# Performance work log

Measured on AMD Instinct MI355X. Metric: run time of the kernel, lower is better.

## Reference

```python
import jax, jax.numpy as jnp
import numpy as np

N = 100000      # num nodes
E = 1600000     # random edges
F_IN = 128      # n_features
H1, H2 = 128, 64   # gnns_forward_hidden
FC1, C = 128, 10   # linears_hidden[-1], n_classes
M = 20000       # masked nodes
SLOPE = 0.2     # LeakyReLU negative slope (GATConv default)


def _glorot(key, shape):
    fan = shape[0]
    return jax.random.normal(key, shape, dtype=jnp.float32) / jnp.sqrt(jnp.float32(fan))


def setup_inputs() -> dict:
    key = jax.random.key(0)
    ks = jax.random.split(key, 16)
    x = jax.random.normal(ks[0], (N, F_IN), dtype=jnp.float32)
    edge_index = jax.random.randint(ks[1], (2, E), 0, N, dtype=jnp.int64)
    mask = jax.random.randint(ks[2], (M,), 0, N, dtype=jnp.int64)
    return {
        "x": x, "edge_index": edge_index, "mask": mask,
        # GAT layer 1: F_IN -> H1
        "W1": _glorot(ks[3], (F_IN, H1)),
        "a_src1": _glorot(ks[4], (H1,)), "a_dst1": _glorot(ks[5], (H1,)),
        "b1": jnp.zeros((H1,), jnp.float32),
        # GAT layer 2: H1 -> H2
        "W2": _glorot(ks[6], (H1, H2)),
        "a_src2": _glorot(ks[7], (H2,)), "a_dst2": _glorot(ks[8], (H2,)),
        "b2": jnp.zeros((H2,), jnp.float32),
        # FC head: H2 -> FC1 -> C
        "fc1_w": _glorot(ks[9], (H2, FC1)), "fc1_b": jnp.zeros((FC1,), jnp.float32),
        "fc2_w": _glorot(ks[10], (FC1, C)), "fc2_b": jnp.zeros((C,), jnp.float32),
    }


def _gat_layer(x, src, dst, W, a_src, a_dst, b):
    h = x @ W                                   # [N, F_out]
    alpha_s = h @ a_src                         # [N]
    alpha_d = h @ a_dst                         # [N]
    e = jax.nn.leaky_relu(alpha_s[src] + alpha_d[dst], SLOPE)  # [E+N]
    # segment softmax over incoming edges of each destination node
    m = jax.ops.segment_max(e, dst, num_segments=N)            # self-loops guarantee non-empty
    w = jnp.exp(e - m[dst])
    z = jax.ops.segment_sum(w, dst, num_segments=N)
    attn = w / z[dst]                           # [E+N]
    out = jax.ops.segment_sum(attn[:, None] * h[src], dst, num_segments=N)
    return out + b


def reference(x, edge_index, mask, W1, a_src1, a_dst1, b1, W2, a_src2, a_dst2, b2, fc1_w, fc1_b, fc2_w, fc2_b):
    loops = jnp.arange(N, dtype=edge_index.dtype)
    src = jnp.concatenate([edge_index[0], loops])   # random edges + self loops (norm_adj adds I)
    dst = jnp.concatenate([edge_index[1], loops])
    h = jax.nn.relu(_gat_layer(x, src, dst, W1, a_src1, a_dst1, b1))   # GATBlock 1 (eval: no dropout/BN)
    h = jax.nn.relu(_gat_layer(h, src, dst, W2, a_src2, a_dst2, b2))   # GATBlock 2
    hm = h[mask]                                    # x[mask] on last layer output
    z = jax.nn.relu(hm @ fc1_w + fc1_b)             # FCsBlock hidden layer
    return z @ fc2_w + fc2_b                        # logits [M, C]
```

## Files before the change

### kernel.cpp

```cpp
#include <hip/hip_runtime.h>
#include <hip/hip_bf16.h>

constexpr int kN    = 100000;
constexpr int kE    = 1600000;
constexpr int kTotE = kE + kN;
constexpr int kM    = 20000;
constexpr float kSlope = 0.2f;

constexpr int kNB   = (kN + 127) >> 7;
constexpr int kBCap = 3072;
constexpr int kEB   = 4096;
constexpr int kSB   = (kTotE + kEB - 1) / kEB;
constexpr int kG1B  = (kN / 16 + 3) / 4;

typedef short short8  __attribute__((ext_vector_type(8)));
typedef float floatx4 __attribute__((ext_vector_type(4)));
typedef float floatx2 __attribute__((ext_vector_type(2)));

__device__ __forceinline__ float bf2f(unsigned short u) {
  union { unsigned int i; float f; } v; v.i = ((unsigned int)u) << 16; return v.f;
}
__device__ __forceinline__ floatx2 ubf2(unsigned int v) {
  union { unsigned int u; float f; } lo, hi;
  lo.u = v << 16; hi.u = v & 0xffff0000u;
  floatx2 r; r.x = lo.f; r.y = hi.f; return r;
}
__device__ __forceinline__ unsigned int packbf2(float lo, float hi) {
  __hip_bfloat162 h = __float22bfloat162_rn(float2{lo, hi});
  union { __hip_bfloat162 v; unsigned int u; } c; c.v = h; return c.u;
}
__device__ __forceinline__ unsigned short f2bf1(float f) {
  return (unsigned short)(packbf2(f, f) & 0xffffu);
}
__device__ __forceinline__ short8 pack8(float4 u, float4 v) {
  union { short8 s; unsigned int w[4]; } r;
  r.w[0] = packbf2(u.x, u.y); r.w[1] = packbf2(u.z, u.w);
  r.w[2] = packbf2(v.x, v.y); r.w[3] = packbf2(v.z, v.w);
  return r.s;
}

__device__ __forceinline__ void wprep1(int idx, const float* W, unsigned short* Wf,
                                       int Fo) {
  int j    = idx & 7;
  int lane = (idx >> 3) & 63;
  int t    = idx >> 9;
  int NT = Fo >> 4;
  int kt = t / NT, nt = t - kt * NT;
  int k = kt * 32 + ((lane >> 4) & 3) * 8 + j;
  int n = nt * 16 + (lane & 15);
  Wf[idx] = f2bf1(W[k * Fo + n]);
}

__global__ __launch_bounds__(256) void k_setup(const float* __restrict__ W1,
                                               const float* __restrict__ W2,
                                               const float* __restrict__ fc1w,
                                               unsigned short* __restrict__ Wf1,
                                               unsigned short* __restrict__ Wf2,
                                               unsigned short* __restrict__ Wf3,
                                               int* __restrict__ bcursor) {
  int gid = blockIdx.x * 256 + threadIdx.x;
  if (gid < kNB) bcursor[gid] = 0;
  if (gid < 16384)      wprep1(gid,          W1,   Wf1, 128);
  else if (gid < 24576) wprep1(gid - 16384,  W2,   Wf2, 64);
  else if (gid < 32768) wprep1(gid - 24576,  fc1w, Wf3, 128);
}

__global__ __launch_bounds__(256) void k_sg1(const int* __restrict__ esrc,
                                             const int* __restrict__ edst,
                                             int* __restrict__ bucketCursor,
                                             int* __restrict__ pairs,
                                             const float* __restrict__ x,
                                             const unsigned short* __restrict__ Wf,
                                             const float* __restrict__ asrc,
                                             const float* __restrict__ adst,
                                             unsigned short* __restrict__ h1,
                                             float* __restrict__ as, float* __restrict__ ad) {
  __shared__ int smemi[4096];
  int t = threadIdx.x;
  if (blockIdx.x < kSB) {
    int* hist    = smemi;
    int* runBase = smemi + kNB;
    int* binCur  = smemi + 2 * kNB;
    int b = blockIdx.x;
    for (int i = t; i < kNB; i += 256) hist[i] = 0;
    __syncthreads();
    int i0 = b * kEB;
#pragma unroll
    for (int k = 0; k < kEB / 256; ++k) {
      int i = i0 + t + k * 256;
      if (i < kTotE) {
        int d = (i < kE) ? edst[i] : (i - kE);
        atomicAdd(&hist[d >> 7], 1);
      }
    }
    __syncthreads();
    for (int i = t; i < kNB; i += 256) {
      int c = hist[i];
      int base = -1;
      if (c) {
        base = atomicAdd(&bucketCursor[i], c);
        if (base + c > kBCap) base = -1;
      }
      runBase[i] = base;
      binCur[i] = 0;
    }
    __syncthreads();
#pragma unroll
    for (int k = 0; k < kEB / 256; ++k) {
      int i = i0 + t + k * 256;
      if (i < kTotE) {
        int s, d;
        if (i < kE) { s = esrc[i]; d = edst[i]; }
        else        { s = d = i - kE; }
        int bin = d >> 7;
        int lp = atomicAdd(&binCur[bin], 1);
        int rb = runBase[bin];
        if (rb >= 0) pairs[(size_t)bin * kBCap + rb + lp] = ((d & 127) << 17) | s;
      }
    }
    return;
  }
  int wave = t >> 6, lane = t & 63;
  int strip = (blockIdx.x - kSB) * 4 + wave;
  if (strip >= kN / 16) return;
  int r0 = strip * 16;
  int m = lane & 15, quad = lane >> 4;
  const float4* xf = (const float4*)(x + (size_t)(r0 + m) * 128);
  short8 a0 = pack8(xf[quad * 2 + 0],  xf[quad * 2 + 1]);
  short8 a1 = pack8(xf[quad * 2 + 8],  xf[quad * 2 + 9]);
  short8 a2 = pack8(xf[quad * 2 + 16], xf[quad * 2 + 17]);
  short8 a3 = pack8(xf[quad * 2 + 24], xf[quad * 2 + 25]);
  const short8* wf = (const short8*)Wf;
  floatx4 acc[8];
#pragma unroll
  for (int nt = 0; nt < 8; ++nt) acc[nt] = floatx4{0.f, 0.f, 0.f, 0.f};
#pragma unroll
  for (int nt = 0; nt < 8; ++nt) {
    acc[nt] = __builtin_amdgcn_mfma_f32_16x16x32_bf16(a0, wf[(0 * 8 + nt) * 64 + lane], acc[nt], 0, 0, 0);
    acc[nt] = __builtin_amdgcn_mfma_f32_16x16x32_bf16(a1, wf[(1 * 8 + nt) * 64 + lane], acc[nt], 0, 0, 0);
    acc[nt] = __builtin_amdgcn_mfma_f32_16x16x32_bf16(a2, wf[(2 * 8 + nt) * 64 + lane], acc[nt], 0, 0, 0);
    acc[nt] = __builtin_amdgcn_mfma_f32_16x16x32_bf16(a3, wf[(3 * 8 + nt) * 64 + lane], acc[nt], 0, 0, 0);
  }
#pragma unroll
  for (int reg = 0; reg < 4; ++reg) {
    float s = 0.f, d = 0.f;
#pragma unroll
    for (int nt = 0; nt < 8; ++nt) {
      float v = acc[nt][reg];
      s += v * asrc[nt * 16 + m];
      d += v * adst[nt * 16 + m];
    }
#pragma unroll
    for (int off = 1; off < 16; off <<= 1) { s += __shfl_xor(s, off); d += __shfl_xor(d, off); }
    if (m == 0) { as[r0 + quad * 4 + reg] = s; ad[r0 + quad * 4 + reg] = d; }
  }
  unsigned short* tw = (unsigned short*)smemi + wave * 2048;
#pragma unroll
  for (int nt = 0; nt < 8; ++nt)
#pragma unroll
    for (int reg = 0; reg < 4; ++reg)
      tw[(quad * 4 + reg) * 128 + nt * 16 + m] = f2bf1(acc[nt][reg]);
  asm volatile("s_waitcnt lgkmcnt(0)" ::: "memory");
  const short8* tr = (const short8*)tw;
  short8* dstp = (short8*)(h1 + (size_t)r0 * 128);
#pragma unroll
  for (int sweep = 0; sweep < 4; ++sweep)
    dstp[sweep * 64 + lane] = tr[sweep * 64 + lane];
}

__global__ __launch_bounds__(256) void k_bucket_csr(int* __restrict__ pairs,
                                                    const int* __restrict__ bucketCursor,
                                                    int* __restrict__ rstart,
                                                    int* __restrict__ degA) {
  __shared__ int pl[kBCap];
  __shared__ int colLDS[kBCap];
  __shared__ int nhist[128], nstart[128], ncur[128], scanbuf[128];
  int b = blockIdx.x, t = threadIdx.x;
  int cnt  = min(bucketCursor[b], kBCap);
  int base = b * kBCap;
  if (t < 128) { nhist[t] = 0; ncur[t] = 0; }
  __syncthreads();
  for (int j = t; j < cnt; j += 256) {
    int p = pairs[(size_t)base + j];
    pl[j] = p;
    atomicAdd(&nhist[(p >> 17) & 127], 1);
  }
  __syncthreads();
  if (t < 128) scanbuf[t] = nhist[t];
  __syncthreads();
  for (int off = 1; off < 128; off <<= 1) {
    int u = (t < 128 && t >= off) ? scanbuf[t - off] : 0;
    __syncthreads();
    if (t < 128) scanbuf[t] += u;
    __syncthreads();
  }
  if (t < 128) nstart[t] = scanbuf[t] - nhist[t];
  __syncthreads();
  int nodes = min(128, kN - b * 128);
  if (t < nodes) {
    rstart[b * 128 + t] = base + nstart[t];
    degA[b * 128 + t]   = nhist[t];
  }
  for (int j = t; j < cnt; j += 256) {
    int p = pl[j];
    int nl = (p >> 17) & 127;
    int lp = atomicAdd(&ncur[nl], 1);
    colLDS[nstart[nl] + lp] = p & 0x1FFFF;
  }
  __syncthreads();
  for (int j = t; j < cnt; j += 256)
    pairs[(size_t)base + j] = colLDS[j];
}

__global__ __launch_bounds__(256) void k_gemm2(const unsigned short* __restrict__ o1,
                                               const unsigned short* __restrict__ Wf,
                                               const float* __restrict__ asrc,
                                               const float* __restrict__ adst,
                                               unsigned short* __restrict__ h2,
                                               float* __restrict__ as, float* __restrict__ ad) {
  __shared__ unsigned short tile[4][16 * 64];
  int wave = threadIdx.x >> 6, lane = threadIdx.x & 63;
  int strip = blockIdx.x * 4 + wave;
  if (strip >= kN / 16) return;
  int r0 = strip * 16;
  int m = lane & 15, quad = lane >> 4;
  const short8* xs = (const short8*)(o1 + (size_t)(r0 + m) * 128);
  short8 a0 = xs[quad], a1 = xs[quad + 4], a2 = xs[quad + 8], a3 = xs[quad + 12];
  const short8* wf = (const short8*)Wf;
  floatx4 acc[4];
#pragma unroll
  for (int nt = 0; nt < 4; ++nt) acc[nt] = floatx4{0.f, 0.f, 0.f, 0.f};
#pragma unroll
  for (int nt = 0; nt < 4; ++nt) {
    acc[nt] = __builtin_amdgcn_mfma_f32_16x16x32_bf16(a0, wf[(0 * 4 + nt) * 64 + lane], acc[nt], 0, 0, 0);
    acc[nt] = __builtin_amdgcn_mfma_f32_16x16x32_bf16(a1, wf[(1 * 4 + nt) * 64 + lane], acc[nt], 0, 0, 0);
    acc[nt] = __builtin_amdgcn_mfma_f32_16x16x32_bf16(a2, wf[(2 * 4 + nt) * 64 + lane], acc[nt], 0, 0, 0);
    acc[nt] = __builtin_amdgcn_mfma_f32_16x16x32_bf16(a3, wf[(3 * 4 + nt) * 64 + lane], acc[nt], 0, 0, 0);
  }
#pragma unroll
  for (int reg = 0; reg < 4; ++reg) {
    float s = 0.f, d = 0.f;
#pragma unroll
    for (int nt = 0; nt < 4; ++nt) {
      float v = acc[nt][reg];
      s += v * asrc[nt * 16 + m];
      d += v * adst[nt * 16 + m];
    }
#pragma unroll
    for (int off = 1; off < 16; off <<= 1) { s += __shfl_xor(s, off); d += __shfl_xor(d, off); }
    if (m == 0) { as[r0 + quad * 4 + reg] = s; ad[r0 + quad * 4 + reg] = d; }
  }
  unsigned short* tw = tile[wave];
#pragma unroll
  for (int nt = 0; nt < 4; ++nt)
#pragma unroll
    for (int reg = 0; reg < 4; ++reg)
      tw[(quad * 4 + reg) * 64 + nt * 16 + m] = f2bf1(acc[nt][reg]);
  asm volatile("s_waitcnt lgkmcnt(0)" ::: "memory");
  const short8* tr = (const short8*)tw;
  short8* dstp = (short8*)(h2 + (size_t)r0 * 64);
#pragma unroll
  for (int sweep = 0; sweep < 2; ++sweep)
    dstp[sweep * 64 + lane] = tr[sweep * 64 + lane];
}

template <int F, bool MASKED>
__global__ __launch_bounds__(256) void k_agg(const unsigned short* __restrict__ h,
                                             const int* __restrict__ rstart,
                                             const int* __restrict__ degA,
                                             const int* __restrict__ col,
                                             const float* __restrict__ as,
                                             const float* __restrict__ ad,
                                             const float* __restrict__ bias,
                                             unsigned short* __restrict__ out,
                                             const int* __restrict__ maskIdx) {
  __shared__ int2 swb[4][64];
  int wave = threadIdx.x >> 6, lane = threadIdx.x & 63;
  int idx = blockIdx.x * 4 + wave;
  if (idx >= (MASKED ? kM : kN)) return;
  int n = MASKED ? maskIdx[idx] : idx;
  int nout = MASKED ? idx : n;
  int beg = rstart[n];
  int deg = degA[n];
  float adn = ad[n];

  if (deg <= 64) {
    int j = beg + lane;
    int boff = 0; float e = -1e30f;
    if (lane < deg) {
      int s = col[j];
      boff = s << (F == 128 ? 8 : 7);
      float t = as[s] + adn;
      e = t > 0.f ? t : kSlope * t;
    }
    float mx = e;
#pragma unroll
    for (int off = 32; off; off >>= 1) mx = fmaxf(mx, __shfl_xor(mx, off));
    float w0 = __expf(e - mx);
    float l = w0;
#pragma unroll
    for (int off = 32; off; off >>= 1) l += __shfl_xor(l, off);
    float w = w0 * (1.f / l);
    floatx2 ax0{0.f, 0.f}, ax1{0.f, 0.f}, ax2{0.f, 0.f}, ax3{0.f, 0.f};
    const char* hb = (const char*)h;
    if (F == 128) {
      int quarter = lane >> 4, ql = lane & 15;
      int cnt8 = (deg + 7) & ~7;
#pragma unroll 2
      for (int k = 0; k < cnt8; k += 8) {
        int i1 = k + quarter, i2 = i1 + 4;
        int   b1 = __shfl(boff, i1), b2 = __shfl(boff, i2);
        float w1 = __shfl(w, i1),    w2 = __shfl(w, i2);
        uint4 v1 = *(const uint4*)(hb + b1 + ql * 16);
        uint4 v2 = *(const uint4*)(hb + b2 + ql * 16);
        floatx2 wv1{w1, w1}, wv2{w2, w2};
        ax0 += wv1 * ubf2(v1.x); ax1 += wv1 * ubf2(v1.y);
        ax2 += wv1 * ubf2(v1.z); ax3 += wv1 * ubf2(v1.w);
        ax0 += wv2 * ubf2(v2.x); ax1 += wv2 * ubf2(v2.y);
        ax2 += wv2 * ubf2(v2.z); ax3 += wv2 * ubf2(v2.w);
      }
      float a[8] = {ax0.x, ax0.y, ax1.x, ax1.y, ax2.x, ax2.y, ax3.x, ax3.y};
#pragma unroll
      for (int i = 0; i < 8; ++i) {
        a[i] += __shfl_xor(a[i], 16);
        a[i] += __shfl_xor(a[i], 32);
      }
      if (quarter == 0) {
        float4 b0 = ((const float4*)bias)[ql * 2];
        float4 b1 = ((const float4*)bias)[ql * 2 + 1];
        uint4 pk;
        pk.x = packbf2(fmaxf(a[0] + b0.x, 0.f), fmaxf(a[1] + b0.y, 0.f));
        pk.y = packbf2(fmaxf(a[2] + b0.z, 0.f), fmaxf(a[3] + b0.w, 0.f));
        pk.z = packbf2(fmaxf(a[4] + b1.x, 0.f), fmaxf(a[5] + b1.y, 0.f));
        pk.w = packbf2(fmaxf(a[6] + b1.z, 0.f), fmaxf(a[7] + b1.w, 0.f));
        ((uint4*)(out + (size_t)nout * 128))[ql] = pk;
      }
    } else {
      int eighth = lane >> 3, el = lane & 7;
      int cnt16 = (deg + 15) & ~15;
#pragma unroll 2
      for (int k = 0; k < cnt16; k += 16) {
        int i1 = k + eighth, i2 = i1 + 8;
        int   b1 = __shfl(boff, i1), b2 = __shfl(boff, i2);
        float w1 = __shfl(w, i1),    w2 = __shfl(w, i2);
        uint4 v1 = *(const uint4*)(hb + b1 + el * 16);
        uint4 v2 = *(const uint4*)(hb + b2 + el * 16);
        floatx2 wv1{w1, w1}, wv2{w2, w2};
        ax0 += wv1 * ubf2(v1.x); ax1 += wv1 * ubf2(v1.y);
        ax2 += wv1 * ubf2(v1.z); ax3 += wv1 * ubf2(v1.w);
        ax0 += wv2 * ubf2(v2.x); ax1 += wv2 * ubf2(v2.y);
        ax2 += wv2 * ubf2(v2.z); ax3 += wv2 * ubf2(v2.w);
      }
      float a[8] = {ax0.x, ax0.y, ax1.x, ax1.y, ax2.x, ax2.y, ax3.x, ax3.y};
#pragma unroll
      for (int i = 0; i < 8; ++i) {
        a[i] += __shfl_xor(a[i], 8);
        a[i] += __shfl_xor(a[i], 16);
        a[i] += __shfl_xor(a[i], 32);
      }
      if (eighth == 0) {
        float4 b0 = ((const float4*)bias)[el * 2];
        float4 b1 = ((const float4*)bias)[el * 2 + 1];
        uint4 pk;
        pk.x = packbf2(fmaxf(a[0] + b0.x, 0.f), fmaxf(a[1] + b0.y, 0.f));
        pk.y = packbf2(fmaxf(a[2] + b0.z, 0.f), fmaxf(a[3] + b0.w, 0.f));
        pk.z = packbf2(fmaxf(a[4] + b1.x, 0.f), fmaxf(a[5] + b1.y, 0.f));
        pk.w = packbf2(fmaxf(a[6] + b1.z, 0.f), fmaxf(a[7] + b1.w, 0.f));
        ((uint4*)(out + (size_t)nout * 64))[el] = pk;
      }
    }
    return;
  }

  int end = beg + deg;
  float m = -1e30f, l = 0.f;
  for (int j0 = beg; j0 < end; j0 += 64) {
    int j = j0 + lane;
    float e = -1e30f;
    if (j < end) {
      int s = col[j];
      float t = as[s] + adn;
      e = t > 0.f ? t : kSlope * t;
    }
    float cm = e;
#pragma unroll
    for (int off = 32; off; off >>= 1) cm = fmaxf(cm, __shfl_xor(cm, off));
    float w = __expf(e - cm);
    float cl = w;
#pragma unroll
    for (int off = 32; off; off >>= 1) cl += __shfl_xor(cl, off);
    float mn = fmaxf(m, cm);
    l = l * __expf(m - mn) + cl * __expf(cm - mn);
    m = mn;
  }
  float invl = 1.f / l;
  float a0 = 0.f, a1 = 0.f;
  int half = lane >> 5, hl = lane & 31;
  for (int j0 = beg; j0 < end; j0 += 64) {
    asm volatile("s_waitcnt lgkmcnt(0)" ::: "memory");
    int j = j0 + lane;
    if (j < end) {
      int s = col[j];
      float t = as[s] + adn;
      float e = t > 0.f ? t : kSlope * t;
      float w = __expf(e - m) * invl;
      swb[wave][lane] = int2{s, (int)__float_as_int(w)};
    }
    asm volatile("s_waitcnt lgkmcnt(0)" ::: "memory");
    int cntc = min(64, end - j0);
    if (F == 128) {
      for (int k = 0; k < cntc; ++k) {
        int2 p = swb[wave][k];
        float w = __int_as_float(p.y);
        unsigned int v = ((const unsigned int*)(h + (size_t)p.x * 128))[lane];
        a0 += w * bf2f((unsigned short)(v & 0xffffu));
        a1 += w * bf2f((unsigned short)(v >> 16));
      }
    } else {
      for (int k = 0; k < cntc; k += 2) {
        int kk = k + half;
        if (kk < cntc) {
          int2 p = swb[wave][kk];
          float w = __int_as_float(p.y);
          unsigned int v = ((const unsigned int*)(h + (size_t)p.x * 64))[hl];
          a0 += w * bf2f((unsigned short)(v & 0xffffu));
          a1 += w * bf2f((unsigned short)(v >> 16));
        }
      }
    }
  }
  if (F == 128) {
    float o0 = fmaxf(a0 + bias[2 * lane], 0.f);
    float o1 = fmaxf(a1 + bias[2 * lane + 1], 0.f);
    ((unsigned int*)(out + (size_t)nout * 128))[lane] = packbf2(o0, o1);
  } else {
    a0 += __shfl_xor(a0, 32);
    a1 += __shfl_xor(a1, 32);
    if (half == 0) {
      float o0 = fmaxf(a0 + bias[2 * hl], 0.f);
      float o1 = fmaxf(a1 + bias[2 * hl + 1], 0.f);
      ((unsigned int*)(out + (size_t)nout * 64))[hl] = packbf2(o0, o1);
    }
  }
}

__global__ __launch_bounds__(256) void k_fc(const unsigned short* __restrict__ o2m,
                                            const unsigned short* __restrict__ Wf,
                                            const float* __restrict__ fc1b,
                                            const float* __restrict__ fc2w,
                                            const float* __restrict__ fc2b,
                                            float* __restrict__ out) {
  __shared__ unsigned short tile[4][16 * 128];
  int wave = threadIdx.x >> 6, lane = threadIdx.x & 63;
  int strip = blockIdx.x * 4 + wave;
  if (strip >= kM / 16) return;
  int r0 = strip * 16;
  int m = lane & 15, quad = lane >> 4;
  const short8* xs = (const short8*)(o2m + (size_t)(r0 + m) * 64);
  short8 a0 = xs[quad], a1 = xs[quad + 4];
  const short8* wf = (const short8*)Wf;
  floatx4 acc[8];
#pragma unroll
  for (int nt = 0; nt < 8; ++nt) acc[nt] = floatx4{0.f, 0.f, 0.f, 0.f};
#pragma unroll
  for (int nt = 0; nt < 8; ++nt) {
    acc[nt] = __builtin_amdgcn_mfma_f32_16x16x32_bf16(a0, wf[(0 * 8 + nt) * 64 + lane], acc[nt], 0, 0, 0);
    acc[nt] = __builtin_amdgcn_mfma_f32_16x16x32_bf16(a1, wf[(1 * 8 + nt) * 64 + lane], acc[nt], 0, 0, 0);
  }
  unsigned short* tw = tile[wave];
#pragma unroll
  for (int nt = 0; nt < 8; ++nt) {
    float bb = fc1b[nt * 16 + m];
#pragma unroll
    for (int reg = 0; reg < 4; ++reg)
      tw[(quad * 4 + reg) * 128 + nt * 16 + m] = f2bf1(fmaxf(acc[nt][reg] + bb, 0.f));
  }
  asm volatile("s_waitcnt lgkmcnt(0)" ::: "memory");
  int c = lane & 15, q = lane >> 4;
  bool active = c < 10;
  float wreg[32];
#pragma unroll
  for (int i = 0; i < 32; ++i)
    wreg[i] = active ? fc2w[(q * 32 + i) * 10 + c] : 0.f;
  float bc = active ? fc2b[c] : 0.f;
  for (int r = 0; r < 16; ++r) {
    const uint2* zr = (const uint2*)(tw + r * 128 + q * 32);
    float acc2 = 0.f;
#pragma unroll
    for (int i = 0; i < 8; ++i) {
      uint2 v = zr[i];
      acc2 += bf2f((unsigned short)(v.x & 0xffffu)) * wreg[4 * i]
            + bf2f((unsigned short)(v.x >> 16))     * wreg[4 * i + 1]
            + bf2f((unsigned short)(v.y & 0xffffu)) * wreg[4 * i + 2]
            + bf2f((unsigned short)(v.y >> 16))     * wreg[4 * i + 3];
    }
    acc2 += __shfl_xor(acc2, 16);
    acc2 += __shfl_xor(acc2, 32);
    if (q == 0 && active) out[(size_t)(r0 + r) * 10 + c] = acc2 + bc;
  }
}

extern "C" void kernel_launch(void* const* d_in, const int* in_sizes, int n_in,
                              void* d_out, int out_size, void* d_ws, size_t ws_size,
                              hipStream_t stream) {
  const float* x     = (const float*)d_in[0];
  const int*   ei    = (const int*)d_in[1];
  const int*   mask  = (const int*)d_in[2];
  const float* W1    = (const float*)d_in[3];
  const float* asrc1 = (const float*)d_in[4];
  const float* adst1 = (const float*)d_in[5];
  const float* b1    = (const float*)d_in[6];
  const float* W2    = (const float*)d_in[7];
  const float* asrc2 = (const float*)d_in[8];
  const float* adst2 = (const float*)d_in[9];
  const float* b2    = (const float*)d_in[10];
  const float* fc1w  = (const float*)d_in[11];
  const float* fc1b  = (const float*)d_in[12];
  const float* fc2w  = (const float*)d_in[13];
  const float* fc2b  = (const float*)d_in[14];
  float* out = (float*)d_out;

  const int* esrc = ei;
  const int* edst = ei + kE;

  char* ws = (char*)d_ws;
  size_t off = 0;
  auto alloc = [&](size_t bytes) -> void* {
    void* p = ws + off;
    off = (off + bytes + 255) & ~(size_t)255;
    return p;
  };
  unsigned short* Wf1     = (unsigned short*)alloc(128 * 128 * 2);
  unsigned short* Wf2     = (unsigned short*)alloc(128 * 64 * 2);
  unsigned short* Wf3     = (unsigned short*)alloc(64 * 128 * 2);
  int*            rstart  = (int*)alloc((size_t)kN * 4);
  int*            degA    = (int*)alloc((size_t)kN * 4);
  int*            bcursor = (int*)alloc((size_t)kNB * 4);
  float*          as1     = (float*)alloc((size_t)kN * 4);
  float*          ad1     = (float*)alloc((size_t)kN * 4);
  float*          as2     = (float*)alloc((size_t)kN * 4);
  float*          ad2     = (float*)alloc((size_t)kN * 4);
  int*            pairs   = (int*)alloc((size_t)kNB * kBCap * 4);
  unsigned short* h1      = (unsigned short*)alloc((size_t)kN * 128 * 2);
  unsigned short* o1      = (unsigned short*)alloc((size_t)kN * 128 * 2);
  unsigned short* h2  = h1;
  unsigned short* o2m = h1 + (size_t)kN * 64;
  (void)ws_size; (void)in_sizes; (void)n_in; (void)out_size;

  const int nodeBlocks = (kN + 3) / 4;
  const int maskBlocks = (kM + 3) / 4;

  k_setup<<<128, 256, 0, stream>>>(W1, W2, fc1w, Wf1, Wf2, Wf3, bcursor);
  k_sg1<<<kSB + kG1B, 256, 0, stream>>>(esrc, edst, bcursor, pairs,
                                        x, Wf1, asrc1, adst1, h1, as1, ad1);
  k_bucket_csr<<<kNB, 256, 0, stream>>>(pairs, bcursor, rstart, degA);
  k_agg<128, false><<<nodeBlocks, 256, 0, stream>>>(h1, rstart, degA, pairs,
                                                    as1, ad1, b1, o1, nullptr);
  k_gemm2<<<kG1B, 256, 0, stream>>>(o1, Wf2, asrc2, adst2, h2, as2, ad2);
  k_agg<64, true><<<maskBlocks, 256, 0, stream>>>(h2, rstart, degA, pairs,
                                                  as2, ad2, b2, o2m, mask);
  k_fc<<<(kM / 16 + 3) / 4, 256, 0, stream>>>(o2m, Wf3, fc1b, fc2w, fc2b, out);
}
```

Baseline: 266.6 us.

## Slice layer-1 features into column blocks and precompute softmax weights in CSR build

The layer-1 GEMM now writes h1 in a sliced layout: 8 feature slices of 16 bf16 each, stored contiguously across nodes. A new slice-parallel aggregation kernel gathers only 32 bytes per edge per block, which aims to keep each slice's working set cache-resident during the random gather. The per-edge attention softmax for layer 1 moves into the bucket CSR kernel, computed serially per node into a new weights buffer. Each edge's col and weight are then re-read eight times, and the softmax runs one thread per node, which risks load imbalance and extra memory traffic.

```diff
diff --git a/kernel.cpp b/kernel.cpp
--- a/kernel.cpp
+++ b/kernel.cpp
@@ -162,16 +162,23 @@
       tw[(quad * 4 + reg) * 128 + nt * 16 + m] = f2bf1(acc[nt][reg]);
   asm volatile("s_waitcnt lgkmcnt(0)" ::: "memory");
   const short8* tr = (const short8*)tw;
-  short8* dstp = (short8*)(h1 + (size_t)r0 * 128);
-#pragma unroll
-  for (int sweep = 0; sweep < 4; ++sweep)
-    dstp[sweep * 64 + lane] = tr[sweep * 64 + lane];
+  short8* h8 = (short8*)h1;
+#pragma unroll
+  for (int sweep = 0; sweep < 4; ++sweep) {
+    int i8 = sweep * 64 + lane;
+    int row = i8 >> 4, e8 = i8 & 15;
+    int slice = e8 >> 1, half = e8 & 1;
+    h8[((size_t)slice * kN + (r0 + row)) * 2 + half] = tr[i8];
+  }
 }
 
 __global__ __launch_bounds__(256) void k_bucket_csr(int* __restrict__ pairs,
                                                     const int* __restrict__ bucketCursor,
                                                     int* __restrict__ rstart,
-                                                    int* __restrict__ degA) {
+                                                    int* __restrict__ degA,
+                                                    const float* __restrict__ as1,
+                                                    const float* __restrict__ ad1,
+                                                    float* __restrict__ wts) {
   __shared__ int pl[kBCap];
   __shared__ int colLDS[kBCap];
   __shared__ int nhist[128], nstart[128], ncur[128], scanbuf[128];
@@ -210,6 +217,66 @@
   __syncthreads();
   for (int j = t; j < cnt; j += 256)
     pairs[(size_t)base + j] = colLDS[j];
+  float* eLDS = (float*)pl;
+  if (t < nodes) {
+    int st = nstart[t], dg = nhist[t];
+    float adn = ad1[b * 128 + t];
+    float mx = -1e30f;
+    for (int i = 0; i < dg; ++i) {
+      int s = colLDS[st + i];
+      float tt = as1[s] + adn;
+      float e = tt > 0.f ? tt : kSlope * tt;
+      eLDS[st + i] = e;
+      mx = fmaxf(mx, e);
+    }
+    float sum = 0.f;
+    for (int i = 0; i < dg; ++i) sum += __expf(eLDS[st + i] - mx);
+    float inv = 1.f / sum;
+    for (int i = 0; i < dg; ++i)
+      wts[(size_t)base + st + i] = __expf(eLDS[st + i] - mx) * inv;
+  }
+}
+
+__global__ __launch_bounds__(256) void k_aggs(const unsigned short* __restrict__ h1s,
+                                              const int* __restrict__ rstart,
+                                              const int* __restrict__ degA,
+                                              const int* __restrict__ col,
+                                              const float* __restrict__ wts,
+                                              const float* __restrict__ bias,
+                                              unsigned short* __restrict__ o1) {
+  int slice = blockIdx.x & 7;
+  int group = blockIdx.x >> 3;
+  int wave = threadIdx.x >> 6, lane = threadIdx.x & 63;
+  int n = group * 4 + wave;
+  if (n >= kN) return;
+  int beg = rstart[n], deg = degA[n];
+  int eg = lane >> 2, fl = lane & 3;
+  const char* hb = (const char*)h1s + (size_t)slice * kN * 32 + fl * 8;
+  floatx2 ax0{0.f, 0.f}, ax1{0.f, 0.f};
+  for (int k = 0; k < deg; k += 16) {
+    int e = k + eg;
+    if (e < deg) {
+      int s = col[beg + e];
+      float w = wts[beg + e];
+      uint2 v = *(const uint2*)(hb + (size_t)s * 32);
+      floatx2 wv{w, w};
+      ax0 += wv * ubf2(v.x);
+      ax1 += wv * ubf2(v.y);
+    }
+  }
+  float a0 = ax0.x, a1 = ax0.y, a2 = ax1.x, a3 = ax1.y;
+#pragma unroll
+  for (int off = 4; off < 64; off <<= 1) {
+    a0 += __shfl_xor(a0, off); a1 += __shfl_xor(a1, off);
+    a2 += __shfl_xor(a2, off); a3 += __shfl_xor(a3, off);
+  }
+  if (eg == 0) {
+    float4 bb = ((const float4*)bias)[slice * 4 + fl];
+    uint2 pk;
+    pk.x = packbf2(fmaxf(a0 + bb.x, 0.f), fmaxf(a1 + bb.y, 0.f));
+    pk.y = packbf2(fmaxf(a2 + bb.z, 0.f), fmaxf(a3 + bb.w, 0.f));
+    *(uint2*)((char*)o1 + (size_t)n * 256 + slice * 32 + fl * 8) = pk;
+  }
 }
 
 __global__ __launch_bounds__(256) void k_gemm2(const unsigned short* __restrict__ o1,
@@ -264,22 +331,21 @@
     dstp[sweep * 64 + lane] = tr[sweep * 64 + lane];
 }
 
-template <int F, bool MASKED>
-__global__ __launch_bounds__(256) void k_agg(const unsigned short* __restrict__ h,
-                                             const int* __restrict__ rstart,
-                                             const int* __restrict__ degA,
-                                             const int* __restrict__ col,
-                                             const float* __restrict__ as,
-                                             const float* __restrict__ ad,
-                                             const float* __restrict__ bias,
-                                             unsigned short* __restrict__ out,
-                                             const int* __restrict__ maskIdx) {
+__global__ __launch_bounds__(256) void k_agg64(const unsigned short* __restrict__ h,
+                                               const int* __restrict__ rstart,
+                                               const int* __restrict__ degA,
+                                               const int* __restrict__ col,
+                                               const float* __restrict__ as,
+                                               const float* __restrict__ ad,
+                                               const float* __restrict__ bias,
+                                               unsigned short* __restrict__ out,
+                                               const int* __restrict__ maskIdx) {
   __shared__ int2 swb[4][64];
   int wave = threadIdx.x >> 6, lane = threadIdx.x & 63;
   int idx = blockIdx.x * 4 + wave;
-  if (idx >= (MASKED ? kM : kN)) return;
-  int n = MASKED ? maskIdx[idx] : idx;
-  int nout = MASKED ? idx : n;
+  if (idx >= kM) return;
+  int n = maskIdx[idx];
+  int nout = idx;
   int beg = rstart[n];
   int deg = degA[n];
   float adn = ad[n];
@@ -289,7 +355,7 @@
     int boff = 0; float e = -1e30f;
     if (lane < deg) {
       int s = col[j];
-      boff = s << (F == 128 ? 8 : 7);
+      boff = s << 7;
       float t = as[s] + adn;
       e = t > 0.f ? t : kSlope * t;
     }
@@ -303,71 +369,37 @@
     float w = w0 * (1.f / l);
     floatx2 ax0{0.f, 0.f}, ax1{0.f, 0.f}, ax2{0.f, 0.f}, ax3{0.f, 0.f};
     const char* hb = (const char*)h;
-    if (F == 128) {
-      int quarter = lane >> 4, ql = lane & 15;
-      int cnt8 = (deg + 7) & ~7;
+    int eighth = lane >> 3, el = lane & 7;
+    int cnt16 = (deg + 15) & ~15;
 #pragma unroll 2
-      for (int k = 0; k < cnt8; k += 8) {
-        int i1 = k + quarter, i2 = i1 + 4;
-        int   b1 = __shfl(boff, i1), b2 = __shfl(boff, i2);
-        float w1 = __shfl(w, i1),    w2 = __shfl(w, i2);
-        uint4 v1 = *(const uint4*)(hb + b1 + ql * 16);
-        uint4 v2 = *(const uint4*)(hb + b2 + ql * 16);
-        floatx2 wv1{w1, w1}, wv2{w2, w2};
-        ax0 += wv1 * ubf2(v1.x); ax1 += wv1 * ubf2(v1.y);
-        ax2 += wv1 * ubf2(v1.z); ax3 += wv1 * ubf2(v1.w);
-        ax0 += wv2 * ubf2(v2.x); ax1 += wv2 * ubf2(v2.y);
-        ax2 += wv2 * ubf2(v2.z); ax3 += wv2 * ubf2(v2.w);
-      }
-      float a[8] = {ax0.x, ax0.y, ax1.x, ax1.y, ax2.x, ax2.y, ax3.x, ax3.y};
-#pragma unroll
-      for (int i = 0; i < 8; ++i) {
-        a[i] += __shfl_xor(a[i], 16);
-        a[i] += __shfl_xor(a[i], 32);
-      }
-      if (quarter == 0) {
-        float4 b0 = ((const float4*)bias)[ql * 2];
-        float4 b1 = ((const float4*)bias)[ql * 2 + 1];
-        uint4 pk;
-        pk.x = packbf2(fmaxf(a[0] + b0.x, 0.f), fmaxf(a[1] + b0.y, 0.f));
-        pk.y = packbf2(fmaxf(a[2] + b0.z, 0.f), fmaxf(a[3] + b0.w, 0.f));
-        pk.z = packbf2(fmaxf(a[4] + b1.x, 0.f), fmaxf(a[5] + b1.y, 0.f));
-        pk.w = packbf2(fmaxf(a[6] + b1.z, 0.f), fmaxf(a[7] + b1.w, 0.f));
-        ((uint4*)(out + (size_t)nout * 128))[ql] = pk;
-      }
-    } else {
-      int eighth = lane >> 3, el = lane & 7;
-      int cnt16 = (deg + 15) & ~15;
-#pragma unroll 2
-      for (int k = 0; k < cnt16; k += 16) {
-        int i1 = k + eighth, i2 = i1 + 8;
-        int   b1 = __shfl(boff, i1), b2 = __shfl(boff, i2);
-        float w1 = __shfl(w, i1),    w2 = __shfl(w, i2);
-        uint4 v1 = *(const uint4*)(hb + b1 + el * 16);
-        uint4 v2 = *(const uint4*)(hb + b2 + el * 16);
-        floatx2 wv1{w1, w1}, wv2{w2, w2};
-        ax0 += wv1 * ubf2(v1.x); ax1 += wv1 * ubf2(v1.y);
-        ax2 += wv1 * ubf2(v1.z); ax3 += wv1 * ubf2(v1.w);
-        ax0 += wv2 * ubf2(v2.x); ax1 += wv2 * ubf2(v2.y);
-        ax2 += wv2 * ubf2(v2.z); ax3 += wv2 * ubf2(v2.w);
-      }
-      float a[8] = {ax0.x, ax0.y, ax1.x, ax1.y, ax2.x, ax2.y, ax3.x, ax3.y};
-#pragma unroll
-      for (int i = 0; i < 8; ++i) {
-        a[i] += __shfl_xor(a[i], 8);
-        a[i] += __shfl_xor(a[i], 16);
-        a[i] += __shfl_xor(a[i], 32);
-      }
-      if (eighth == 0) {
-        float4 b0 = ((const float4*)bias)[el * 2];
-        float4 b1 = ((const float4*)bias)[el * 2 + 1];
-        uint4 pk;
-        pk.x = packbf2(fmaxf(a[0] + b0.x, 0.f), fmaxf(a[1] + b0.y, 0.f));
-        pk.y = packbf2(fmaxf(a[2] + b0.z, 0.f), fmaxf(a[3] + b0.w, 0.f));
-        pk.z = packbf2(fmaxf(a[4] + b1.x, 0.f), fmaxf(a[5] + b1.y, 0.f));
-        pk.w = packbf2(fmaxf(a[6] + b1.z, 0.f), fmaxf(a[7] + b1.w, 0.f));
-        ((uint4*)(out + (size_t)nout * 64))[el] = pk;
-      }
+    for (int k = 0; k < cnt16; k += 16) {
+      int i1 = k + eighth, i2 = i1 + 8;
+      int   b1 = __shfl(boff, i1), b2 = __shfl(boff, i2);
+      float w1 = __shfl(w, i1),    w2 = __shfl(w, i2);
+      uint4 v1 = *(const uint4*)(hb + b1 + el * 16);
+      uint4 v2 = *(const uint4*)(hb + b2 + el * 16);
+      floatx2 wv1{w1, w1}, wv2{w2, w2};
+      ax0 += wv1 * ubf2(v1.x); ax1 += wv1 * ubf2(v1.y);
+      ax2 += wv1 * ubf2(v1.z); ax3 += wv1 * ubf2(v1.w);
+      ax0 += wv2 * ubf2(v2.x); ax1 += wv2 * ubf2(v2.y);
+      ax2 += wv2 * ubf2(v2.z); ax3 += wv2 * ubf2(v2.w);
+    }
+    float a[8] = {ax0.x, ax0.y, ax1.x, ax1.y, ax2.x, ax2.y, ax3.x, ax3.y};
+#pragma unroll
+    for (int i = 0; i < 8; ++i) {
+      a[i] += __shfl_xor(a[i], 8);
+      a[i] += __shfl_xor(a[i], 16);
+      a[i] += __shfl_xor(a[i], 32);
+    }
+    if (eighth == 0) {
+      float4 b0 = ((const float4*)bias)[el * 2];
+      float4 b1 = ((const float4*)bias)[el * 2 + 1];
+      uint4 pk;
+      pk.x = packbf2(fmaxf(a[0] + b0.x, 0.f), fmaxf(a[1] + b0.y, 0.f));
+      pk.y = packbf2(fmaxf(a[2] + b0.z, 0.f), fmaxf(a[3] + b0.w, 0.f));
+      pk.z = packbf2(fmaxf(a[4] + b1.x, 0.f), fmaxf(a[5] + b1.y, 0.f));
+      pk.w = packbf2(fmaxf(a[6] + b1.z, 0.f), fmaxf(a[7] + b1.w, 0.f));
+      ((uint4*)(out + (size_t)nout * 64))[el] = pk;
     }
     return;
   }
@@ -408,39 +440,23 @@
     }
     asm volatile("s_waitcnt lgkmcnt(0)" ::: "memory");
     int cntc = min(64, end - j0);
-    if (F == 128) {
-      for (int k = 0; k < cntc; ++k) {
-        int2 p = swb[wave][k];
+    for (int k = 0; k < cntc; k += 2) {
+      int kk = k + half;
+      if (kk < cntc) {
+        int2 p = swb[wave][kk];
         float w = __int_as_float(p.y);
-        unsigned int v = ((const unsigned int*)(h + (size_t)p.x * 128))[lane];
+        unsigned int v = ((const unsigned int*)(h + (size_t)p.x * 64))[hl];
         a0 += w * bf2f((unsigned short)(v & 0xffffu));
         a1 += w * bf2f((unsigned short)(v >> 16));
       }
-    } else {
-      for (int k = 0; k < cntc; k += 2) {
-        int kk = k + half;
-        if (kk < cntc) {
-          int2 p = swb[wave][kk];
-          float w = __int_as_float(p.y);
-          unsigned int v = ((const unsigned int*)(h + (size_t)p.x * 64))[hl];
-          a0 += w * bf2f((unsigned short)(v & 0xffffu));
-          a1 += w * bf2f((unsigned short)(v >> 16));
-        }
-      }
-    }
-  }
-  if (F == 128) {
-    float o0 = fmaxf(a0 + bias[2 * lane], 0.f);
-    float o1 = fmaxf(a1 + bias[2 * lane + 1], 0.f);
-    ((unsigned int*)(out + (size_t)nout * 128))[lane] = packbf2(o0, o1);
-  } else {
-    a0 += __shfl_xor(a0, 32);
-    a1 += __shfl_xor(a1, 32);
-    if (half == 0) {
-      float o0 = fmaxf(a0 + bias[2 * hl], 0.f);
-      float o1 = fmaxf(a1 + bias[2 * hl + 1], 0.f);
-      ((unsigned int*)(out + (size_t)nout * 64))[hl] = packbf2(o0, o1);
-    }
+    }
+  }
+  a0 += __shfl_xor(a0, 32);
+  a1 += __shfl_xor(a1, 32);
+  if (half == 0) {
+    float o0 = fmaxf(a0 + bias[2 * hl], 0.f);
+    float o1 = fmaxf(a1 + bias[2 * hl + 1], 0.f);
+    ((unsigned int*)(out + (size_t)nout * 64))[hl] = packbf2(o0, o1);
   }
 }
 
@@ -541,23 +557,22 @@
   float*          as2     = (float*)alloc((size_t)kN * 4);
   float*          ad2     = (float*)alloc((size_t)kN * 4);
   int*            pairs   = (int*)alloc((size_t)kNB * kBCap * 4);
+  float*          wts     = (float*)alloc((size_t)kNB * kBCap * 4);
   unsigned short* h1      = (unsigned short*)alloc((size_t)kN * 128 * 2);
   unsigned short* o1      = (unsigned short*)alloc((size_t)kN * 128 * 2);
   unsigned short* h2  = h1;
   unsigned short* o2m = h1 + (size_t)kN * 64;
   (void)ws_size; (void)in_sizes; (void)n_in; (void)out_size;
 
-  const int nodeBlocks = (kN + 3) / 4;
   const int maskBlocks = (kM + 3) / 4;
 
   k_setup<<<128, 256, 0, stream>>>(W1, W2, fc1w, Wf1, Wf2, Wf3, bcursor);
   k_sg1<<<kSB + kG1B, 256, 0, stream>>>(esrc, edst, bcursor, pairs,
                                         x, Wf1, asrc1, adst1, h1, as1, ad1);
-  k_bucket_csr<<<kNB, 256, 0, stream>>>(pairs, bcursor, rstart, degA);
-  k_agg<128, false><<<nodeBlocks, 256, 0, stream>>>(h1, rstart, degA, pairs,
-                                                    as1, ad1, b1, o1, nullptr);
+  k_bucket_csr<<<kNB, 256, 0, stream>>>(pairs, bcursor, rstart, degA, as1, ad1, wts);
+  k_aggs<<<((kN + 3) / 4) * 8, 256, 0, stream>>>(h1, rstart, degA, pairs, wts, b1, o1);
   k_gemm2<<<kG1B, 256, 0, stream>>>(o1, Wf2, asrc2, adst2, h2, as2, ad2);
-  k_agg<64, true><<<maskBlocks, 256, 0, stream>>>(h2, rstart, degA, pairs,
-                                                  as2, ad2, b2, o2m, mask);
+  k_agg64<<<maskBlocks, 256, 0, stream>>>(h2, rstart, degA, pairs,
+                                          as2, ad2, b2, o2m, mask);
   k_fc<<<(kM / 16 + 3) / 4, 256, 0, stream>>>(o2m, Wf3, fc1b, fc2w, fc2b, out);
 }
```

Result: slower. 462.2 us (+73.4%).
